# Performance work log

Hardware: AMD Instinct MI355X
Metric: run time of the kernel (lower is better)

Reference implementation:

```python
import jax, jax.numpy as jnp
import numpy as np

EPS = 1e-6
NEG = 1e9

def _norm(x):
    # Normalizator math with alpha=1, gamma=0 (torch.std is unbiased -> ddof=1)
    m = jnp.mean(x, axis=-1, keepdims=True)
    s = jnp.std(x, axis=-1, ddof=1, keepdims=True)
    return (x - m) / (s + EPS)

def setup_inputs() -> dict:
    key = jax.random.key(0)
    ks = jax.random.split(key, 16)
    T, S, D, F, L = 4096, 4096, 512, 2048, 4
    sc = 1.0 / np.sqrt(D)
    scf = 1.0 / np.sqrt(F)
    return {
        "current_tgt_output": jax.random.normal(ks[0], (T, D), jnp.float32),
        "encoder_output": jax.random.normal(ks[1], (S, D), jnp.float32),
        "cross_mask": jax.random.randint(ks[2], (T, S), 0, 2).astype(jnp.float32),
        "Wq": jax.random.normal(ks[3], (L, D, D), jnp.float32) * sc,
        "Wk": jax.random.normal(ks[4], (L, D, D), jnp.float32) * sc,
        "Wv": jax.random.normal(ks[5], (L, D, D), jnp.float32) * sc,
        "Wo": jax.random.normal(ks[6], (L, D, D), jnp.float32) * sc,
        "Cq": jax.random.normal(ks[7], (L, D, D), jnp.float32) * sc,
        "Ck": jax.random.normal(ks[8], (L, D, D), jnp.float32) * sc,
        "Cv": jax.random.normal(ks[9], (L, D, D), jnp.float32) * sc,
        "Co": jax.random.normal(ks[10], (L, D, D), jnp.float32) * sc,
        "W1": jax.random.normal(ks[11], (L, D, F), jnp.float32) * sc,
        "W2": jax.random.normal(ks[12], (L, F, D), jnp.float32) * scf,
        "alpha": jnp.ones((1,), jnp.float32),
        "gamma": jnp.zeros((1,), jnp.float32),
        "input_ids": jax.random.randint(ks[13], (T,), 0, S),
        "training_step": T,
        "training_mode": 1,
    }

def reference(current_tgt_output, encoder_output, cross_mask, Wq, Wk, Wv, Wo,
              Cq, Ck, Cv, Co, W1, W2, alpha, gamma, input_ids,
              training_step, training_mode):
    T = training_step
    x = current_tgt_output[:T] if training_mode else current_tgt_output
    cm = cross_mask[:T]                                  # [T, S]
    # the python double-loop -> single vectorized gather: self_mask[i,k]=cross_mask[i, input_ids[k]]
    self_mask = cm[:, input_ids]                         # [T, T]
    sbias = (self_mask - 1.0) * NEG                      # additive mask bias
    cbias = (cm - 1.0) * NEG
    D = x.shape[-1]
    scale = 1.0 / jnp.sqrt(jnp.asarray(D, x.dtype))
    L = Wq.shape[0]
    for l in range(L):
        h = _norm(x)
        q, k, v = h @ Wq[l], h @ Wk[l], h @ Wv[l]
        a = jax.nn.softmax(q @ k.T * scale + sbias, axis=-1)
        x = x + (a @ v) @ Wo[l]
        h = _norm(x)
        q = h @ Cq[l]
        k, v = encoder_output @ Ck[l], encoder_output @ Cv[l]
        a = jax.nn.softmax(q @ k.T * scale + cbias, axis=-1)
        x = x + (a @ v) @ Co[l]
        h = _norm(x)
        x = x + jax.nn.relu(h @ W1[l]) @ W2[l]
    return alpha * _norm(x) + gamma
```

## Files before the change

kernel.cpp:

```cpp
#include <hip/hip_runtime.h>
#include <math.h>

typedef _Float16 half_t;
typedef unsigned int u32;
typedef unsigned short u16;
typedef float f32x4 __attribute__((ext_vector_type(4)));
typedef _Float16 f16x8 __attribute__((ext_vector_type(8)));
typedef _Float16 f16x4 __attribute__((ext_vector_type(4)));

#define T_DIM 4096
#define S_DIM 4096
#define D_DIM 512
#define F_DIM 2048
#define NLAYER 4

__device__ __forceinline__ void gload16(const void* g, void* l) {
    __builtin_amdgcn_global_load_lds(
        (const __attribute__((address_space(1))) u32*)g,
        (__attribute__((address_space(3))) u32*)l, 16, 0, 0);
}

template<int N> __device__ __forceinline__ void wait_vm() {
    if constexpr (N == 0) asm volatile("s_waitcnt vmcnt(0)" ::: "memory");
    else if constexpr (N == 3) asm volatile("s_waitcnt vmcnt(3)" ::: "memory");
    else if constexpr (N == 4) asm volatile("s_waitcnt vmcnt(4)" ::: "memory");
    else if constexpr (N == 6) asm volatile("s_waitcnt vmcnt(6)" ::: "memory");
    else if constexpr (N == 8) asm volatile("s_waitcnt vmcnt(8)" ::: "memory");
}

template<int BN, int EPI, int SPLITK = 1>
__global__ __launch_bounds__(512)
void gemm_nt(const half_t* __restrict__ A, int lda,
             const half_t* __restrict__ B, int ldb,
             int N, int K, int gx,
             const float* __restrict__ Cin, float* __restrict__ Cout,
             half_t* __restrict__ D1, half_t* __restrict__ D2,
             half_t* __restrict__ D3, int ldd)
{
    constexpr int BM = 128, BK = 64;
    constexpr int NF = BN / 32;
    constexpr int LPT = 2 + BN / 64;
    constexpr int NSLOT = (BN == 64) ? 3 : 2;
    __shared__ half_t As[NSLOT][BM * BK];
    __shared__ half_t Bs[NSLOT][BN * BK];

    const int tid  = threadIdx.x;
    const int wave = tid >> 6;
    const int lane = tid & 63;

    const int nb  = gridDim.x;
    const int bid = blockIdx.x;
    const int nid = (bid & 7) * (nb >> 3) + (bid >> 3);
    const int gy  = nb / (gx * SPLITK);
    const int bx  = nid % gx;
    const int tmp = nid / gx;
    const int by  = tmp % gy;
    const int kz  = tmp / gy;
    const int bm = by * BM, bn = bx * BN;

    const int Keff = K / SPLITK;
    A += (size_t)kz * Keff;
    B += (size_t)kz * Keff;

    const int wm = (wave >> 1) * 32;
    const int wn = (wave & 1) * (BN / 2);
    const int kq = lane >> 4;
    const int rr = lane & 15;
    const int scol = (((lane & 7) ^ (lane >> 3)) << 3);

    f32x4 acc[2][NF];
#pragma unroll
    for (int m = 0; m < 2; ++m)
#pragma unroll
        for (int n = 0; n < NF; ++n)
            acc[m][n] = f32x4{0.f, 0.f, 0.f, 0.f};

    auto stage = [&](int buf, int k0) {
#pragma unroll
        for (int c = 0; c < 2; ++c) {
            const int row = wave * 16 + c * 8 + (lane >> 3);
            gload16(A + (size_t)(bm + row) * lda + k0 + scol,
                    (char*)&As[buf][0] + (wave * 2 + c) * 1024 + lane * 16);
        }
        if constexpr (BN == 64) {
            const int row = wave * 8 + (lane >> 3);
            gload16(B + (size_t)(bn + row) * ldb + k0 + scol,
                    (char*)&Bs[buf][0] + wave * 1024 + lane * 16);
        } else {
#pragma unroll
            for (int c = 0; c < 2; ++c) {
                const int row = wave * 16 + c * 8 + (lane >> 3);
                gload16(B + (size_t)(bn + row) * ldb + k0 + scol,
                        (char*)&Bs[buf][0] + (wave * 2 + c) * 1024 + lane * 16);
            }
        }
    };

    const int nt = Keff / BK;
    stage(0, 0);
    if constexpr (NSLOT == 3) stage(1, BK);
    int cur = 0, pf = NSLOT - 1;
    for (int t = 0; t < nt; ++t) {
        if (t + 1 < nt) wait_vm<(NSLOT - 2) * LPT>(); else wait_vm<0>();
        __builtin_amdgcn_s_barrier();
        if (t + NSLOT - 1 < nt) stage(pf, (t + NSLOT - 1) * BK);
#pragma unroll
        for (int ks = 0; ks < 2; ++ks) {
            f16x8 af[2], bf[NF];
#pragma unroll
            for (int m = 0; m < 2; ++m) {
                const int r = wm + m * 16 + rr;
                af[m] = *(const f16x8*)&As[cur][r * BK + (((ks * 4 + kq) ^ (r & 7)) << 3)];
            }
#pragma unroll
            for (int n = 0; n < NF; ++n) {
                const int r = wn + n * 16 + rr;
                bf[n] = *(const f16x8*)&Bs[cur][r * BK + (((ks * 4 + kq) ^ (r & 7)) << 3)];
            }
#pragma unroll
            for (int m = 0; m < 2; ++m)
#pragma unroll
                for (int n = 0; n < NF; ++n)
                    acc[m][n] = __builtin_amdgcn_mfma_f32_16x16x32_f16(af[m], bf[n], acc[m][n], 0, 0, 0);
        }
        cur = (cur + 1 == NSLOT) ? 0 : cur + 1;
        pf  = (pf  + 1 == NSLOT) ? 0 : pf  + 1;
    }

    const int r0 = bm + wm + (lane >> 4) * 4;
#pragma unroll
    for (int m = 0; m < 2; ++m)
#pragma unroll
        for (int n = 0; n < NF; ++n) {
            const int c = bn + wn + n * 16 + rr;
            if constexpr (SPLITK > 1) {
                float* Cp = Cout + (size_t)kz * gy * BM * N;
#pragma unroll
                for (int i = 0; i < 4; ++i)
                    Cp[(size_t)(r0 + m * 16 + i) * N + c] = acc[m][n][i];
            } else if (EPI == 0 || EPI == 1) {
#pragma unroll
                for (int i = 0; i < 4; ++i) {
                    const int r = r0 + m * 16 + i;
                    const float v = acc[m][n][i];
                    Cout[(size_t)r * N + c] = (EPI == 1) ? (Cin[(size_t)r * N + c] + v) : v;
                }
            } else if (EPI == 2 || EPI == 4) {
#pragma unroll
                for (int i = 0; i < 4; ++i) {
                    float v = acc[m][n][i];
                    if (EPI == 4) v = fmaxf(v, 0.f);
                    D1[(size_t)(r0 + m * 16 + i) * ldd + c] = (half_t)v;
                }
            } else if (EPI == 3) {
                f16x4 hv;
#pragma unroll
                for (int i = 0; i < 4; ++i) hv[i] = (half_t)acc[m][n][i];
                *(f16x4*)&D1[(size_t)c * ldd + r0 + m * 16] = hv;
            } else if (EPI == 5) {
                if (bn < 512) {
#pragma unroll
                    for (int i = 0; i < 4; ++i)
                        D1[(size_t)(r0 + m * 16 + i) * 512 + c] = (half_t)acc[m][n][i];
                } else if (bn < 1024) {
#pragma unroll
                    for (int i = 0; i < 4; ++i)
                        D2[(size_t)(r0 + m * 16 + i) * 512 + (c - 512)] = (half_t)acc[m][n][i];
                } else {
                    f16x4 hv;
#pragma unroll
                    for (int i = 0; i < 4; ++i) hv[i] = (half_t)acc[m][n][i];
                    *(f16x4*)&D3[(size_t)(c - 1024) * ldd + r0 + m * 16] = hv;
                }
            } else {
                if (bn < 512) {
#pragma unroll
                    for (int i = 0; i < 4; ++i)
                        D2[(size_t)(r0 + m * 16 + i) * 512 + c] = (half_t)acc[m][n][i];
                } else {
                    f16x4 hv;
#pragma unroll
                    for (int i = 0; i < 4; ++i) hv[i] = (half_t)acc[m][n][i];
                    *(f16x4*)&D3[(size_t)(c - 512) * ldd + r0 + m * 16] = hv;
                }
            }
        }
}

template<int NS, int MODE>
__global__ __launch_bounds__(256)
void reduce_splitk(const float* __restrict__ P, const float* __restrict__ Cin,
                   float* __restrict__ Cout, half_t* __restrict__ D)
{
    const size_t MN = (size_t)T_DIM * 512;
    const size_t i = ((size_t)blockIdx.x * 256 + threadIdx.x) * 8;
    float s[8];
    {
        float4 a = *(const float4*)&P[i];
        float4 b = *(const float4*)&P[i + 4];
        s[0] = a.x; s[1] = a.y; s[2] = a.z; s[3] = a.w;
        s[4] = b.x; s[5] = b.y; s[6] = b.z; s[7] = b.w;
    }
#pragma unroll
    for (int k = 1; k < NS; ++k) {
        float4 a = *(const float4*)&P[k * MN + i];
        float4 b = *(const float4*)&P[k * MN + i + 4];
        s[0] += a.x; s[1] += a.y; s[2] += a.z; s[3] += a.w;
        s[4] += b.x; s[5] += b.y; s[6] += b.z; s[7] += b.w;
    }
    if (MODE == 0) {
        f16x8 o;
#pragma unroll
        for (int j = 0; j < 8; ++j) o[j] = (half_t)s[j];
        *(f16x8*)&D[i] = o;
    } else {
        float4 c0 = *(const float4*)&Cin[i];
        float4 c1 = *(const float4*)&Cin[i + 4];
        float4 o0 = {c0.x + s[0], c0.y + s[1], c0.z + s[2], c0.w + s[3]};
        float4 o1 = {c1.x + s[4], c1.y + s[5], c1.z + s[6], c1.w + s[7]};
        *(float4*)&Cout[i] = o0;
        *(float4*)&Cout[i + 4] = o1;
    }
}

template<int FINAL>
__global__ __launch_bounds__(256)
void norm_rows(const float* __restrict__ x, half_t* __restrict__ hh,
               float* __restrict__ outF, const float* __restrict__ alphaP,
               const float* __restrict__ gammaP)
{
    const int row  = blockIdx.x * 4 + (threadIdx.x >> 6);
    const int lane = threadIdx.x & 63;
    const float* xr = x + (size_t)row * D_DIM + lane * 8;
    float4 a = *(const float4*)xr;
    float4 b = *(const float4*)(xr + 4);
    float v[8] = {a.x, a.y, a.z, a.w, b.x, b.y, b.z, b.w};
    float s = 0.f;
#pragma unroll
    for (int j = 0; j < 8; ++j) s += v[j];
#pragma unroll
    for (int off = 32; off; off >>= 1) s += __shfl_xor(s, off);
    const float mean = s * (1.f / 512.f);
    float ss = 0.f;
#pragma unroll
    for (int j = 0; j < 8; ++j) { float d = v[j] - mean; ss += d * d; }
#pragma unroll
    for (int off = 32; off; off >>= 1) ss += __shfl_xor(ss, off);
    const float inv = 1.f / (sqrtf(ss * (1.f / 511.f)) + 1e-6f);
    if (FINAL) {
        const float alp = alphaP[0], gam = gammaP[0];
        float o[8];
#pragma unroll
        for (int j = 0; j < 8; ++j) o[j] = alp * ((v[j] - mean) * inv) + gam;
        float4 o0 = {o[0], o[1], o[2], o[3]};
        float4 o1 = {o[4], o[5], o[6], o[7]};
        float* op = outF + (size_t)row * D_DIM + lane * 8;
        *(float4*)op = o0;
        *(float4*)(op + 4) = o1;
    } else {
        f16x8 hv;
#pragma unroll
        for (int j = 0; j < 8; ++j) hv[j] = (half_t)((v[j] - mean) * inv);
        *(f16x8*)&hh[(size_t)row * D_DIM + lane * 8] = hv;
    }
}

__global__ __launch_bounds__(256)
void cast_f16(const float* __restrict__ in, half_t* __restrict__ out)
{
    size_t i = ((size_t)blockIdx.x * 256 + threadIdx.x) * 8;
    float4 a = *(const float4*)&in[i];
    float4 b = *(const float4*)&in[i + 4];
    float v[8] = {a.x, a.y, a.z, a.w, b.x, b.y, b.z, b.w};
    f16x8 o;
#pragma unroll
    for (int j = 0; j < 8; ++j) o[j] = (half_t)v[j];
    *(f16x8*)&out[i] = o;
}

__global__ __launch_bounds__(256)
void transpose_cast(const float* __restrict__ in, half_t* __restrict__ out,
                    int R, int C, float scale, int inZ, int outZ)
{
    in  += (size_t)blockIdx.z * inZ;
    out += (size_t)blockIdx.z * outZ;
    __shared__ float tile[32][33];
    const int tx = threadIdx.x & 31, ty = threadIdx.x >> 5;
    const int r0 = blockIdx.y * 32, c0 = blockIdx.x * 32;
#pragma unroll
    for (int i = 0; i < 4; ++i)
        tile[ty + i * 8][tx] = in[(size_t)(r0 + ty + i * 8) * C + c0 + tx];
    __syncthreads();
#pragma unroll
    for (int i = 0; i < 4; ++i)
        out[(size_t)(c0 + ty + i * 8) * R + r0 + tx] = (half_t)(tile[tx][ty + i * 8] * scale);
}

__global__ __launch_bounds__(256)
void pack_masks(const float* __restrict__ cm, const int* __restrict__ ids,
                u32* __restrict__ crossb, u32* __restrict__ selfb)
{
    const int t = blockIdx.x;
    const float* row = cm + (size_t)t * S_DIM;
    __shared__ u32 cb[S_DIM / 32];
    __shared__ u16 sh16[256];
    const int tid = threadIdx.x;
    u32 bits = 0;
#pragma unroll
    for (int q = 0; q < 4; ++q) {
        float4 v = *(const float4*)&row[tid * 16 + q * 4];
        bits |= (v.x > 0.5f ? 1u : 0u) << (q * 4 + 0);
        bits |= (v.y > 0.5f ? 1u : 0u) << (q * 4 + 1);
        bits |= (v.z > 0.5f ? 1u : 0u) << (q * 4 + 2);
        bits |= (v.w > 0.5f ? 1u : 0u) << (q * 4 + 3);
    }
    ((u16*)cb)[tid] = (u16)bits;
    __syncthreads();
    u32 sb = 0;
#pragma unroll
    for (int q = 0; q < 4; ++q) {
        int4 id4 = *(const int4*)&ids[tid * 16 + q * 4];
        sb |= ((cb[id4.x >> 5] >> (id4.x & 31)) & 1u) << (q * 4 + 0);
        sb |= ((cb[id4.y >> 5] >> (id4.y & 31)) & 1u) << (q * 4 + 1);
        sb |= ((cb[id4.z >> 5] >> (id4.z & 31)) & 1u) << (q * 4 + 2);
        sb |= ((cb[id4.w >> 5] >> (id4.w & 31)) & 1u) << (q * 4 + 3);
    }
    sh16[tid] = (u16)sb;
    __syncthreads();
    if (tid < 128) {
        crossb[(size_t)t * 128 + tid] = cb[tid];
        selfb[(size_t)t * 128 + tid]  = (u32)sh16[2 * tid] | ((u32)sh16[2 * tid + 1] << 16);
    }
}

__global__ __launch_bounds__(256)
void softmax_rows(float* __restrict__ logits, const u32* __restrict__ bits)
{
    const int t = blockIdx.x;
    float* row = logits + (size_t)t * S_DIM;
    const u32* bw = bits + (size_t)t * (S_DIM / 32);
    __shared__ float red[8];
    const int tid = threadIdx.x, wave = tid >> 6, lane = tid & 63;
    float z[16];
    float lmax = -3.0e38f;
#pragma unroll
    for (int j = 0; j < 4; ++j) {
        const int s = j * 1024 + tid * 4;
        float4 v = *(const float4*)&row[s];
        const u32 w = bw[s >> 5];
        const int sh = s & 31;
        z[j * 4 + 0] = v.x + (((w >> (sh + 0)) & 1u) ? 0.f : -1e9f);
        z[j * 4 + 1] = v.y + (((w >> (sh + 1)) & 1u) ? 0.f : -1e9f);
        z[j * 4 + 2] = v.z + (((w >> (sh + 2)) & 1u) ? 0.f : -1e9f);
        z[j * 4 + 3] = v.w + (((w >> (sh + 3)) & 1u) ? 0.f : -1e9f);
        lmax = fmaxf(lmax, fmaxf(fmaxf(z[j*4], z[j*4+1]), fmaxf(z[j*4+2], z[j*4+3])));
    }
#pragma unroll
    for (int off = 32; off; off >>= 1) lmax = fmaxf(lmax, __shfl_xor(lmax, off));
    if (lane == 0) red[wave] = lmax;
    __syncthreads();
    const float mx = fmaxf(fmaxf(red[0], red[1]), fmaxf(red[2], red[3]));
    float lsum = 0.f;
#pragma unroll
    for (int q = 0; q < 16; ++q) { z[q] = __expf(z[q] - mx); lsum += z[q]; }
#pragma unroll
    for (int off = 32; off; off >>= 1) lsum += __shfl_xor(lsum, off);
    if (lane == 0) red[4 + wave] = lsum;
    __syncthreads();
    const float inv = 1.f / (red[4] + red[5] + red[6] + red[7]);
    half_t* ph = (half_t*)row;
#pragma unroll
    for (int j = 0; j < 4; ++j) {
        const int s = j * 1024 + tid * 4;
        f16x4 hv;
#pragma unroll
        for (int q = 0; q < 4; ++q) hv[q] = (half_t)(z[j * 4 + q] * inv);
        *(f16x4*)&ph[s] = hv;
    }
}

extern "C" void kernel_launch(void* const* d_in, const int* in_sizes, int n_in,
                              void* d_out, int out_size, void* d_ws, size_t ws_size,
                              hipStream_t stream)
{
    (void)in_sizes; (void)n_in; (void)out_size; (void)ws_size;

    const float* x0p  = (const float*)d_in[0];
    const float* encp = (const float*)d_in[1];
    const float* cmp  = (const float*)d_in[2];
    const float* Wq = (const float*)d_in[3], *Wk = (const float*)d_in[4];
    const float* Wv = (const float*)d_in[5], *Wo = (const float*)d_in[6];
    const float* Cq = (const float*)d_in[7], *Ck = (const float*)d_in[8];
    const float* Cv = (const float*)d_in[9], *Co = (const float*)d_in[10];
    const float* W1p = (const float*)d_in[11];
    const float* W2p = (const float*)d_in[12];
    const float* alphap = (const float*)d_in[13];
    const float* gammap = (const float*)d_in[14];
    const int*   idsp   = (const int*)d_in[15];
    float* outp = (float*)d_out;

    char* wp = (char*)d_ws;
    auto take = [&](size_t nelem, int esz) -> void* {
        void* p = (void*)wp;
        wp += (nelem * (size_t)esz + 255) & ~(size_t)255;
        return p;
    };
    half_t* wqkvT = (half_t*)take((size_t)NLAYER * 1536 * 512, 2);
    half_t* ckvT  = (half_t*)take((size_t)NLAYER * 1024 * 512, 2);
    half_t* cqT   = (half_t*)take((size_t)NLAYER * 512 * 512, 2);
    half_t* woT   = (half_t*)take((size_t)NLAYER * 512 * 512, 2);
    half_t* coT   = (half_t*)take((size_t)NLAYER * 512 * 512, 2);
    half_t* w1T   = (half_t*)take((size_t)NLAYER * D_DIM * F_DIM, 2);
    half_t* w2T   = (half_t*)take((size_t)NLAYER * D_DIM * F_DIM, 2);
    half_t* hh    = (half_t*)take((size_t)T_DIM * D_DIM, 2);
    half_t* qb    = (half_t*)take((size_t)T_DIM * D_DIM, 2);
    half_t* kb    = (half_t*)take((size_t)S_DIM * D_DIM, 2);
    half_t* vT    = (half_t*)take((size_t)S_DIM * D_DIM, 2);
    half_t* ao    = (half_t*)take((size_t)T_DIM * D_DIM, 2);
    half_t* mid   = (half_t*)take((size_t)T_DIM * F_DIM, 2);
    half_t* enc16 = (half_t*)take((size_t)S_DIM * D_DIM, 2);
    float* xbuf   = (float*)take((size_t)T_DIM * D_DIM, 4);
    float* logits = (float*)take((size_t)T_DIM * S_DIM, 4);
    float* pbuf   = (float*)take((size_t)4 * T_DIM * D_DIM, 4);
    u32* crossb = (u32*)take((size_t)T_DIM * (S_DIM / 32), 4);
    u32* selfb  = (u32*)take((size_t)T_DIM * (S_DIM / 32), 4);

    const dim3 B(256), B512(512);
    const float qscale = 0.04419417382415922f;

    const int SQ = 512 * 512, QKVZ = 1536 * 512, KVZ = 1024 * 512, FZ = 512 * 2048;
    transpose_cast<<<dim3(16,16,4), B, 0, stream>>>(Wq, wqkvT,            512, 512, qscale, SQ, QKVZ);
    transpose_cast<<<dim3(16,16,4), B, 0, stream>>>(Wk, wqkvT + SQ,       512, 512, 1.f,    SQ, QKVZ);
    transpose_cast<<<dim3(16,16,4), B, 0, stream>>>(Wv, wqkvT + 2 * SQ,   512, 512, 1.f,    SQ, QKVZ);
    transpose_cast<<<dim3(16,16,4), B, 0, stream>>>(Wo, woT,              512, 512, 1.f,    SQ, SQ);
    transpose_cast<<<dim3(16,16,4), B, 0, stream>>>(Cq, cqT,              512, 512, qscale, SQ, SQ);
    transpose_cast<<<dim3(16,16,4), B, 0, stream>>>(Ck, ckvT,             512, 512, 1.f,    SQ, KVZ);
    transpose_cast<<<dim3(16,16,4), B, 0, stream>>>(Cv, ckvT + SQ,        512, 512, 1.f,    SQ, KVZ);
    transpose_cast<<<dim3(16,16,4), B, 0, stream>>>(Co, coT,              512, 512, 1.f,    SQ, SQ);
    transpose_cast<<<dim3(64,16,4), B, 0, stream>>>(W1p, w1T, 512, 2048, 1.f, FZ, FZ);
    transpose_cast<<<dim3(16,64,4), B, 0, stream>>>(W2p, w2T, 2048, 512, 1.f, FZ, FZ);
    cast_f16<<<dim3((S_DIM * D_DIM / 8) / 256), B, 0, stream>>>(encp, enc16);
    pack_masks<<<dim3(T_DIM), B, 0, stream>>>(cmp, idsp, crossb, selfb);

    const dim3 gRED(T_DIM * D_DIM / 8 / 256);

    for (int l = 0; l < NLAYER; ++l) {
        const float* xin = (l == 0) ? x0p : xbuf;

        norm_rows<0><<<T_DIM / 4, B, 0, stream>>>(xin, hh, nullptr, nullptr, nullptr);
        gemm_nt<64, 5><<<dim3(768), B512, 0, stream>>>(hh, 512, wqkvT + (size_t)l * QKVZ, 512,
            1536, 512, 24, nullptr, nullptr, qb, kb, vT, 4096);
        gemm_nt<128, 0><<<dim3(1024), B512, 0, stream>>>(qb, 512, kb, 512,
            4096, 512, 32, nullptr, logits, nullptr, nullptr, nullptr, 0);
        softmax_rows<<<dim3(T_DIM), B, 0, stream>>>(logits, selfb);
        gemm_nt<64, 0, 4><<<dim3(1024), B512, 0, stream>>>((half_t*)logits, 8192, vT, 4096,
            512, 4096, 8, nullptr, pbuf, nullptr, nullptr, nullptr, 0);
        reduce_splitk<4, 0><<<gRED, B, 0, stream>>>(pbuf, nullptr, nullptr, ao);
        gemm_nt<64, 1><<<dim3(256), B512, 0, stream>>>(ao, 512, woT + (size_t)l * SQ, 512,
            512, 512, 8, xin, xbuf, nullptr, nullptr, nullptr, 0);

        norm_rows<0><<<T_DIM / 4, B, 0, stream>>>(xbuf, hh, nullptr, nullptr, nullptr);
        gemm_nt<64, 2><<<dim3(256), B512, 0, stream>>>(hh, 512, cqT + (size_t)l * SQ, 512,
            512, 512, 8, nullptr, nullptr, qb, nullptr, nullptr, 512);
        gemm_nt<64, 6><<<dim3(512), B512, 0, stream>>>(enc16, 512, ckvT + (size_t)l * KVZ, 512,
            1024, 512, 16, nullptr, nullptr, nullptr, kb, vT, 4096);
        gemm_nt<128, 0><<<dim3(1024), B512, 0, stream>>>(qb, 512, kb, 512,
            4096, 512, 32, nullptr, logits, nullptr, nullptr, nullptr, 0);
        softmax_rows<<<dim3(T_DIM), B, 0, stream>>>(logits, crossb);
        gemm_nt<64, 0, 4><<<dim3(1024), B512, 0, stream>>>((half_t*)logits, 8192, vT, 4096,
            512, 4096, 8, nullptr, pbuf, nullptr, nullptr, nullptr, 0);
        reduce_splitk<4, 0><<<gRED, B, 0, stream>>>(pbuf, nullptr, nullptr, ao);
        gemm_nt<64, 1><<<dim3(256), B512, 0, stream>>>(ao, 512, coT + (size_t)l * SQ, 512,
            512, 512, 8, xbuf, xbuf, nullptr, nullptr, nullptr, 0);

        norm_rows<0><<<T_DIM / 4, B, 0, stream>>>(xbuf, hh, nullptr, nullptr, nullptr);
        gemm_nt<128, 4><<<dim3(512), B512, 0, stream>>>(hh, 512, w1T + (size_t)l * FZ, 512,
            2048, 512, 16, nullptr, nullptr, mid, nullptr, nullptr, 2048);
        gemm_nt<64, 0, 2><<<dim3(512), B512, 0, stream>>>(mid, 2048, w2T + (size_t)l * FZ, 2048,
            512, 2048, 8, nullptr, pbuf, nullptr, nullptr, nullptr, 0);
        reduce_splitk<2, 1><<<gRED, B, 0, stream>>>(pbuf, xbuf, xbuf, nullptr);
    }

    norm_rows<1><<<T_DIM / 4, B, 0, stream>>>(xbuf, nullptr, outp, alphap, gammap);
}
```

Before: 1.198 ms.

## Store attention logits in fp16 and add 256-thread triple-buffered 128x128 GEMM

QK^T logits are now written directly as fp16 from a new 256-thread, 128x128-tile GEMM kernel with three-slot LDS buffering and an XOR-swizzled layout. That GEMM is also used for the FFN up-projection with ReLU. Softmax reads and writes fp16 rows in place, which halves logit traffic versus the fp32 buffer and lets the PV GEMM read a dense fp16 matrix. The trade-off is less precision in the pre-softmax logits, since fp16 range and rounding apply before the mask bias and max subtraction, plus a new GEMM kernel that must beat the tuned one.

```diff
diff --git a/kernel.cpp b/kernel.cpp
--- a/kernel.cpp
+++ b/kernel.cpp
@@ -152,11 +152,6 @@
                     if (EPI == 4) v = fmaxf(v, 0.f);
                     D1[(size_t)(r0 + m * 16 + i) * ldd + c] = (half_t)v;
                 }
-            } else if (EPI == 3) {
-                f16x4 hv;
-#pragma unroll
-                for (int i = 0; i < 4; ++i) hv[i] = (half_t)acc[m][n][i];
-                *(f16x4*)&D1[(size_t)c * ldd + r0 + m * 16] = hv;
             } else if (EPI == 5) {
                 if (bn < 512) {
 #pragma unroll
@@ -183,6 +178,94 @@
                     for (int i = 0; i < 4; ++i) hv[i] = (half_t)acc[m][n][i];
                     *(f16x4*)&D3[(size_t)(c - 512) * ldd + r0 + m * 16] = hv;
                 }
+            }
+        }
+}
+
+template<int EPI>
+__global__ __launch_bounds__(256)
+void gemm97(const half_t* __restrict__ A, int lda,
+            const half_t* __restrict__ B, int ldb,
+            int K, int gx, half_t* __restrict__ D, int ldd)
+{
+    constexpr int BK = 32, NSLOT = 3, LPT = 4;
+    __shared__ half_t As[NSLOT][128 * BK];
+    __shared__ half_t Bs[NSLOT][128 * BK];
+
+    const int tid  = threadIdx.x;
+    const int wave = tid >> 6;
+    const int lane = tid & 63;
+
+    const int nb  = gridDim.x;
+    const int bid = blockIdx.x;
+    const int nid = (bid & 7) * (nb >> 3) + (bid >> 3);
+    const int bx = nid % gx, by = nid / gx;
+    const int bm = by * 128, bn = bx * 128;
+
+    const int wm = (wave >> 1) * 64;
+    const int wn = (wave & 1) * 64;
+    const int kq = lane >> 4;
+    const int rr = lane & 15;
+    const int srow = lane >> 2;
+    const int scol = (((lane & 3) ^ ((lane >> 3) & 3)) << 3);
+    const int kqa  = kq ^ ((rr >> 1) & 3);
+
+    const half_t* Abase = A + (size_t)(bm + wave * 16 + srow) * lda + scol;
+    const half_t* Bbase = B + (size_t)(bn + wave * 16 + srow) * ldb + scol;
+
+    f32x4 acc[4][4];
+#pragma unroll
+    for (int m = 0; m < 4; ++m)
+#pragma unroll
+        for (int n = 0; n < 4; ++n)
+            acc[m][n] = f32x4{0.f, 0.f, 0.f, 0.f};
+
+    auto stage = [&](int buf, int k0) {
+#pragma unroll
+        for (int c = 0; c < 2; ++c)
+            gload16(Abase + (size_t)c * 64 * lda + k0,
+                    (char*)&As[buf][0] + c * 4096 + wave * 1024 + lane * 16);
+#pragma unroll
+        for (int c = 0; c < 2; ++c)
+            gload16(Bbase + (size_t)c * 64 * ldb + k0,
+                    (char*)&Bs[buf][0] + c * 4096 + wave * 1024 + lane * 16);
+    };
+
+    const int nt = K / BK;
+    stage(0, 0);
+    stage(1, BK);
+    int cur = 0, pf = 2;
+    for (int t = 0; t < nt; ++t) {
+        if (t + 1 < nt) wait_vm<LPT>(); else wait_vm<0>();
+        __builtin_amdgcn_s_barrier();
+        if (t + 2 < nt) stage(pf, (t + 2) * BK);
+        f16x8 af[4], bf[4];
+#pragma unroll
+        for (int m = 0; m < 4; ++m)
+            af[m] = *(const f16x8*)&As[cur][(wm + m * 16 + rr) * BK + kqa * 8];
+#pragma unroll
+        for (int n = 0; n < 4; ++n)
+            bf[n] = *(const f16x8*)&Bs[cur][(wn + n * 16 + rr) * BK + kqa * 8];
+#pragma unroll
+        for (int m = 0; m < 4; ++m)
+#pragma unroll
+            for (int n = 0; n < 4; ++n)
+                acc[m][n] = __builtin_amdgcn_mfma_f32_16x16x32_f16(af[m], bf[n], acc[m][n], 0, 0, 0);
+        cur = (cur == 2) ? 0 : cur + 1;
+        pf  = (pf  == 2) ? 0 : pf + 1;
+    }
+
+    const int r0 = bm + wm + (lane >> 4) * 4;
+#pragma unroll
+    for (int m = 0; m < 4; ++m)
+#pragma unroll
+        for (int n = 0; n < 4; ++n) {
+            const int c = bn + wn + n * 16 + rr;
+#pragma unroll
+            for (int i = 0; i < 4; ++i) {
+                float v = acc[m][n][i];
+                if (EPI == 4) v = fmaxf(v, 0.f);
+                D[(size_t)(r0 + m * 16 + i) * ldd + c] = (half_t)v;
             }
         }
 }
@@ -334,26 +417,24 @@
 }
 
 __global__ __launch_bounds__(256)
-void softmax_rows(float* __restrict__ logits, const u32* __restrict__ bits)
+void softmax_rows16(half_t* __restrict__ logits, const u32* __restrict__ bits)
 {
     const int t = blockIdx.x;
-    float* row = logits + (size_t)t * S_DIM;
+    half_t* row = logits + (size_t)t * S_DIM;
     const u32* bw = bits + (size_t)t * (S_DIM / 32);
     __shared__ float red[8];
     const int tid = threadIdx.x, wave = tid >> 6, lane = tid & 63;
+    const int s0 = tid * 16;
+    f16x8 h0 = *(const f16x8*)&row[s0];
+    f16x8 h1 = *(const f16x8*)&row[s0 + 8];
+    const u32 w = bw[tid >> 1] >> ((tid & 1) * 16);
     float z[16];
     float lmax = -3.0e38f;
 #pragma unroll
-    for (int j = 0; j < 4; ++j) {
-        const int s = j * 1024 + tid * 4;
-        float4 v = *(const float4*)&row[s];
-        const u32 w = bw[s >> 5];
-        const int sh = s & 31;
-        z[j * 4 + 0] = v.x + (((w >> (sh + 0)) & 1u) ? 0.f : -1e9f);
-        z[j * 4 + 1] = v.y + (((w >> (sh + 1)) & 1u) ? 0.f : -1e9f);
-        z[j * 4 + 2] = v.z + (((w >> (sh + 2)) & 1u) ? 0.f : -1e9f);
-        z[j * 4 + 3] = v.w + (((w >> (sh + 3)) & 1u) ? 0.f : -1e9f);
-        lmax = fmaxf(lmax, fmaxf(fmaxf(z[j*4], z[j*4+1]), fmaxf(z[j*4+2], z[j*4+3])));
+    for (int q = 0; q < 16; ++q) {
+        const float v = (float)((q < 8) ? h0[q & 7] : h1[q & 7]);
+        z[q] = v + (((w >> q) & 1u) ? 0.f : -1e9f);
+        lmax = fmaxf(lmax, z[q]);
     }
 #pragma unroll
     for (int off = 32; off; off >>= 1) lmax = fmaxf(lmax, __shfl_xor(lmax, off));
@@ -368,15 +449,14 @@
     if (lane == 0) red[4 + wave] = lsum;
     __syncthreads();
     const float inv = 1.f / (red[4] + red[5] + red[6] + red[7]);
-    half_t* ph = (half_t*)row;
-#pragma unroll
-    for (int j = 0; j < 4; ++j) {
-        const int s = j * 1024 + tid * 4;
-        f16x4 hv;
-#pragma unroll
-        for (int q = 0; q < 4; ++q) hv[q] = (half_t)(z[j * 4 + q] * inv);
-        *(f16x4*)&ph[s] = hv;
-    }
+    f16x8 o0, o1;
+#pragma unroll
+    for (int q = 0; q < 8; ++q) {
+        o0[q] = (half_t)(z[q] * inv);
+        o1[q] = (half_t)(z[q + 8] * inv);
+    }
+    *(f16x8*)&row[s0] = o0;
+    *(f16x8*)&row[s0 + 8] = o1;
 }
 
 extern "C" void kernel_launch(void* const* d_in, const int* in_sizes, int n_in,
@@ -420,7 +500,7 @@
     half_t* mid   = (half_t*)take((size_t)T_DIM * F_DIM, 2);
     half_t* enc16 = (half_t*)take((size_t)S_DIM * D_DIM, 2);
     float* xbuf   = (float*)take((size_t)T_DIM * D_DIM, 4);
-    float* logits = (float*)take((size_t)T_DIM * S_DIM, 4);
+    half_t* logit16 = (half_t*)take((size_t)T_DIM * S_DIM, 2);
     float* pbuf   = (float*)take((size_t)4 * T_DIM * D_DIM, 4);
     u32* crossb = (u32*)take((size_t)T_DIM * (S_DIM / 32), 4);
     u32* selfb  = (u32*)take((size_t)T_DIM * (S_DIM / 32), 4);
@@ -450,10 +530,10 @@
         norm_rows<0><<<T_DIM / 4, B, 0, stream>>>(xin, hh, nullptr, nullptr, nullptr);
         gemm_nt<64, 5><<<dim3(768), B512, 0, stream>>>(hh, 512, wqkvT + (size_t)l * QKVZ, 512,
             1536, 512, 24, nullptr, nullptr, qb, kb, vT, 4096);
-        gemm_nt<128, 0><<<dim3(1024), B512, 0, stream>>>(qb, 512, kb, 512,
-            4096, 512, 32, nullptr, logits, nullptr, nullptr, nullptr, 0);
-        softmax_rows<<<dim3(T_DIM), B, 0, stream>>>(logits, selfb);
-        gemm_nt<64, 0, 4><<<dim3(1024), B512, 0, stream>>>((half_t*)logits, 8192, vT, 4096,
+        gemm97<2><<<dim3(1024), B, 0, stream>>>(qb, 512, kb, 512,
+            512, 32, logit16, 4096);
+        softmax_rows16<<<dim3(T_DIM), B, 0, stream>>>(logit16, selfb);
+        gemm_nt<64, 0, 4><<<dim3(1024), B512, 0, stream>>>(logit16, 4096, vT, 4096,
             512, 4096, 8, nullptr, pbuf, nullptr, nullptr, nullptr, 0);
         reduce_splitk<4, 0><<<gRED, B, 0, stream>>>(pbuf, nullptr, nullptr, ao);
         gemm_nt<64, 1><<<dim3(256), B512, 0, stream>>>(ao, 512, woT + (size_t)l * SQ, 512,
@@ -464,18 +544,18 @@
             512, 512, 8, nullptr, nullptr, qb, nullptr, nullptr, 512);
         gemm_nt<64, 6><<<dim3(512), B512, 0, stream>>>(enc16, 512, ckvT + (size_t)l * KVZ, 512,
             1024, 512, 16, nullptr, nullptr, nullptr, kb, vT, 4096);
-        gemm_nt<128, 0><<<dim3(1024), B512, 0, stream>>>(qb, 512, kb, 512,
-            4096, 512, 32, nullptr, logits, nullptr, nullptr, nullptr, 0);
-        softmax_rows<<<dim3(T_DIM), B, 0, stream>>>(logits, crossb);
-        gemm_nt<64, 0, 4><<<dim3(1024), B512, 0, stream>>>((half_t*)logits, 8192, vT, 4096,
+        gemm97<2><<<dim3(1024), B, 0, stream>>>(qb, 512, kb, 512,
+            512, 32, logit16, 4096);
+        softmax_rows16<<<dim3(T_DIM), B, 0, stream>>>(logit16, crossb);
+        gemm_nt<64, 0, 4><<<dim3(1024), B512, 0, stream>>>(logit16, 4096, vT, 4096,
             512, 4096, 8, nullptr, pbuf, nullptr, nullptr, nullptr, 0);
         reduce_splitk<4, 0><<<gRED, B, 0, stream>>>(pbuf, nullptr, nullptr, ao);
         gemm_nt<64, 1><<<dim3(256), B512, 0, stream>>>(ao, 512, coT + (size_t)l * SQ, 512,
             512, 512, 8, xbuf, xbuf, nullptr, nullptr, nullptr, 0);
 
         norm_rows<0><<<T_DIM / 4, B, 0, stream>>>(xbuf, hh, nullptr, nullptr, nullptr);
-        gemm_nt<128, 4><<<dim3(512), B512, 0, stream>>>(hh, 512, w1T + (size_t)l * FZ, 512,
-            2048, 512, 16, nullptr, nullptr, mid, nullptr, nullptr, 2048);
+        gemm97<4><<<dim3(512), B, 0, stream>>>(hh, 512, w1T + (size_t)l * FZ, 512,
+            512, 16, mid, 2048);
         gemm_nt<64, 0, 2><<<dim3(512), B512, 0, stream>>>(mid, 2048, w2T + (size_t)l * FZ, 2048,
             512, 2048, 8, nullptr, pbuf, nullptr, nullptr, nullptr, 0);
         reduce_splitk<2, 1><<<gRED, B, 0, stream>>>(pbuf, xbuf, xbuf, nullptr);
```

After: 1.107 ms. -7.6%, faster.
